# Kernel tuning notes

Hardware: AMD Instinct MI355X
Metric: run time of the kernel (lower is better)

The kernel has to match this reference:

```python
import jax, jax.numpy as jnp
import numpy as np

B = 16384   # batch
F = 26      # categorical fields
N = 100000  # rows per embedding table
M = 16      # embedding dim per field
NUM = 13    # numerical (dense) features
D = F * M + NUM  # embed_output_dim = 429
L = 6       # CrossNet layers (vector parameterization)
H = 1024    # MLP hidden


def setup_inputs() -> dict:
    key = jax.random.key(0)
    ks = jax.random.split(key, 10)
    Xi = jax.random.randint(ks[0], (B, F, 1), 0, N)
    Xv = jax.random.normal(ks[1], (B, NUM), dtype=jnp.float32)
    # per-field tables, init U(-sqrt(1/n), sqrt(1/n)) as in the torch code; stacked flat
    bound = float(np.sqrt(1.0 / N))
    emb_tables = jax.random.uniform(ks[2], (F * N, M), jnp.float32, -bound, bound)
    cross_w = jax.random.normal(ks[3], (L, D), dtype=jnp.float32) * 0.02
    cross_b = jnp.zeros((L, D), dtype=jnp.float32)
    W1 = jax.random.normal(ks[4], (D, H), dtype=jnp.float32) * (1.0 / np.sqrt(D))
    b1 = jnp.zeros((H,), dtype=jnp.float32)
    W2 = jax.random.normal(ks[5], (H, H), dtype=jnp.float32) * (1.0 / np.sqrt(H))
    b2 = jnp.zeros((H,), dtype=jnp.float32)
    Wout = jax.random.normal(ks[6], (H + D, 1), dtype=jnp.float32) * (1.0 / np.sqrt(H + D))
    bout = jnp.zeros((1,), dtype=jnp.float32)
    return dict(Xi=Xi, Xv=Xv, emb_tables=emb_tables, cross_w=cross_w,
                cross_b=cross_b, W1=W1, b1=b1, W2=W2, b2=b2, Wout=Wout, bout=bout)


def reference(Xi, Xv, emb_tables, cross_w, cross_b, W1, b1, W2, b2, Wout, bout):
    # Fused multi-table EmbeddingBag(mode='sum'): one gather over the stacked tables.
    offs = (jnp.arange(F, dtype=Xi.dtype) * N)[None, :, None]        # [1,F,1]
    flat_idx = (Xi + offs).reshape(-1)                               # [B*F*K]
    g = emb_tables[flat_idx].reshape(B, F, -1, M).sum(axis=2)        # [B,F,M] bag-sum
    x0 = jnp.concatenate([Xv, g.reshape(B, F * M)], axis=1)          # [B,D]
    # CrossNet, vector parameterization: x_{l+1} = x0 * (x_l . w_l) + b_l + x_l
    x = x0
    for l in range(L):
        xw = x @ cross_w[l]                                          # [B]
        x = x0 * xw[:, None] + cross_b[l] + x
    # Deep MLP on x0
    h = jax.nn.relu(x0 @ W1 + b1)
    h = jax.nn.relu(h @ W2 + b2)
    out = jnp.concatenate([h, x], axis=1) @ Wout + bout              # [B,1]
    return out[:, 0]
```

## Files before the change

kernel.cpp:

```cpp
#include <hip/hip_runtime.h>
#include <hip/hip_bf16.h>

#define B_   16384
#define F_   26
#define N_   100000
#define M_   16
#define NUM_ 13
#define D_   429
#define KP1_ 448
#define L_   6
#define H_   1024

typedef unsigned short u16;
typedef __bf16 bf16x8 __attribute__((ext_vector_type(8)));
typedef float  f32x4  __attribute__((ext_vector_type(4)));

__device__ __forceinline__ u16 f2bf_bits(float f) {
  union { float f; unsigned u; } x; x.f = f;
  unsigned r = x.u + 0x7FFFu + ((x.u >> 16) & 1u);
  return (u16)(r >> 16);
}

__global__ __launch_bounds__(256) void fused_front(
    const int* __restrict__ Xi, const float* __restrict__ Xv,
    const float* __restrict__ emb,
    const float* __restrict__ cw, const float* __restrict__ cb,
    const float* __restrict__ Wout, const float* __restrict__ bout,
    const float* __restrict__ W1, const float* __restrict__ W2,
    u16* __restrict__ x0b, u16* __restrict__ w1bt, u16* __restrict__ w2bt,
    float* __restrict__ out) {
  __shared__ __align__(16) u16 sbuf[4][KP1_];
  __shared__ __align__(16) float tile[64][68];
  const int blk = blockIdx.x;
  const int tid = threadIdx.x;
  if (blk < B_ / 4) {
    const int w = tid >> 6, lane = tid & 63;
    const int b = blk * 4 + w;
    const int* xi = Xi + b * F_;

    float x0r[7];
    #pragma unroll
    for (int i = 0; i < 7; ++i) {
      int e = i * 64 + lane;
      float v = 0.f;
      if (e < 416) {
        int f = e >> 4;
        int idx = xi[f];
        v = emb[((size_t)f * N_ + idx) * M_ + (e & 15)];
      } else if (e < D_) {
        v = Xv[b * NUM_ + (e - 416)];
      }
      x0r[i] = v;
      sbuf[w][e] = f2bf_bits(v);
    }

    float xr[7];
    #pragma unroll
    for (int i = 0; i < 7; ++i) xr[i] = x0r[i];
    for (int l = 0; l < L_; ++l) {
      float wl[7], bl[7];
      #pragma unroll
      for (int i = 0; i < 7; ++i) {
        int e = i * 64 + lane;
        if (e < D_) {
          int d = (e < 416) ? (13 + e) : (e - 416);
          wl[i] = cw[l * D_ + d]; bl[i] = cb[l * D_ + d];
        } else { wl[i] = 0.f; bl[i] = 0.f; }
      }
      float s = 0.f;
      #pragma unroll
      for (int i = 0; i < 7; ++i) s += xr[i] * wl[i];
      #pragma unroll
      for (int off = 32; off; off >>= 1) s += __shfl_xor(s, off);
      #pragma unroll
      for (int i = 0; i < 7; ++i) xr[i] = x0r[i] * s + bl[i] + xr[i];
    }

    __syncthreads();
    if (lane < 56)
      ((uint4*)(x0b + (size_t)b * KP1_))[lane] = ((const uint4*)sbuf[w])[lane];

    float s = 0.f;
    #pragma unroll
    for (int i = 0; i < 7; ++i) {
      int e = i * 64 + lane;
      if (e < D_) {
        int d = (e < 416) ? (13 + e) : (e - 416);
        s += xr[i] * Wout[H_ + d];
      }
    }
    #pragma unroll
    for (int off = 32; off; off >>= 1) s += __shfl_xor(s, off);
    if (lane == 0) out[b] = s + bout[0];
  } else {
    int pid = blk - B_ / 4;
    if (pid < 112) {
      const int ti = pid >> 4, tj = pid & 15;
      const int e0 = ti * 64, c0 = tj * 64;
      #pragma unroll
      for (int it = 0; it < 4; ++it) {
        int el = it * 16 + (tid >> 4);
        int e = e0 + el;
        int d = (e < 416) ? (13 + e) : ((e < D_) ? (e - 416) : -1);
        float4 v = make_float4(0.f, 0.f, 0.f, 0.f);
        if (d >= 0) v = *(const float4*)&W1[(size_t)d * H_ + c0 + (tid & 15) * 4];
        *(float4*)&tile[el][(tid & 15) * 4] = v;
      }
      __syncthreads();
      const int nl = tid >> 2, ks = (tid & 3) * 16;
      u16 tmp[16];
      #pragma unroll
      for (int x = 0; x < 16; ++x) tmp[x] = f2bf_bits(tile[ks + x][nl]);
      uint4* dst = (uint4*)&w1bt[(size_t)(c0 + nl) * KP1_ + e0 + ks];
      dst[0] = *(uint4*)&tmp[0];
      dst[1] = *(uint4*)&tmp[8];
    } else {
      pid -= 112;
      const int ti = pid >> 4, tj = pid & 15;
      const int k0 = ti * 64, c0 = tj * 64;
      #pragma unroll
      for (int it = 0; it < 4; ++it) {
        int kl = it * 16 + (tid >> 4);
        *(float4*)&tile[kl][(tid & 15) * 4] =
            *(const float4*)&W2[(size_t)(k0 + kl) * H_ + c0 + (tid & 15) * 4];
      }
      __syncthreads();
      const int nl = tid >> 2, ks = (tid & 3) * 16;
      u16 tmp[16];
      #pragma unroll
      for (int x = 0; x < 16; ++x) tmp[x] = f2bf_bits(tile[ks + x][nl]);
      uint4* dst = (uint4*)&w2bt[(size_t)(c0 + nl) * H_ + k0 + ks];
      dst[0] = *(uint4*)&tmp[0];
      dst[1] = *(uint4*)&tmp[8];
    }
  }
}

#define BARR __builtin_amdgcn_s_barrier()
#define VM6  asm volatile("s_waitcnt vmcnt(6)" ::: "memory")
#define VM0  asm volatile("s_waitcnt vmcnt(0)" ::: "memory")
#define MM(ACC) do { \
  __builtin_amdgcn_s_setprio(1); \
  _Pragma("unroll") \
  for (int mi = 0; mi < 4; ++mi) { \
    _Pragma("unroll") \
    for (int ni = 0; ni < 4; ++ni) \
      ACC[mi][ni] = __builtin_amdgcn_mfma_f32_16x16x32_bf16(af[mi], bfc[ni], ACC[mi][ni], 0, 0, 0); \
  } \
  __builtin_amdgcn_s_setprio(0); \
} while (0)

template<int MODE>
__global__ __launch_bounds__(512, 2) void gemm256(
    const u16* __restrict__ A, const u16* __restrict__ BT,
    const float* __restrict__ bias, u16* __restrict__ C,
    const float* __restrict__ Wout, float* __restrict__ out,
    int N, int K) {
  __shared__ __align__(16) u16 As[2][2][256 * 32];
  __shared__ __align__(16) u16 Bs[2][2][256 * 32];
  const int nbx = N >> 8;
  const int cpx = gridDim.x >> 3;
  const int swz = (blockIdx.x & 7) * cpx + (blockIdx.x >> 3);
  const int bx = swz % nbx;
  const int by = swz / nbx;
  const int tid = threadIdx.x;
  const int l = tid & 63;
  const int w = tid >> 6;
  const int wr = w >> 2, wc = w & 3;
  const int nkt = K >> 6;

  const int sr = tid >> 2;
  const int scs = ((tid & 3) ^ ((tid >> 3) & 3)) * 8;
  const u16* gA0 = A  + (size_t)(by * 256 + sr) * K + scs;
  const u16* gB0 = BT + (size_t)(bx * 256 + sr) * K + scs;
  const int dst0 = tid * 8;

  auto stgA = [&](int t, int kk) {
    const u16* s = gA0 + t * 64 + kk * 32;
    __builtin_amdgcn_global_load_lds(
        (const __attribute__((address_space(1))) void*)s,
        (__attribute__((address_space(3))) void*)&As[t & 1][kk][dst0], 16, 0, 0);
    __builtin_amdgcn_global_load_lds(
        (const __attribute__((address_space(1))) void*)(s + (size_t)128 * K),
        (__attribute__((address_space(3))) void*)&As[t & 1][kk][dst0 + 4096], 16, 0, 0);
  };
  auto stgB = [&](int t, int kk) {
    const u16* s = gB0 + t * 64 + kk * 32;
    __builtin_amdgcn_global_load_lds(
        (const __attribute__((address_space(1))) void*)s,
        (__attribute__((address_space(3))) void*)&Bs[t & 1][kk][dst0], 16, 0, 0);
    __builtin_amdgcn_global_load_lds(
        (const __attribute__((address_space(1))) void*)(s + (size_t)128 * K),
        (__attribute__((address_space(3))) void*)&Bs[t & 1][kk][dst0 + 4096], 16, 0, 0);
  };

  const int fr = l & 15, g = l >> 4;
  const int slot = (g ^ ((fr >> 1) & 3)) * 16;
  const int aoff = (wr * 128 + fr) * 64 + slot;
  const int boff = (wc * 64 + fr) * 64 + slot;

  bf16x8 af[4], bfc[4];
  auto rdA = [&](int buf, int kk, int mlo) {
    const char* base = (const char*)&As[buf][kk][0];
    #pragma unroll
    for (int m = 0; m < 4; ++m)
      af[m] = *(const bf16x8*)(base + aoff + (mlo + m) * 1024);
  };
  auto rdB = [&](int buf, int kk) {
    const char* base = (const char*)&Bs[buf][kk][0];
    #pragma unroll
    for (int n = 0; n < 4; ++n)
      bfc[n] = *(const bf16x8*)(base + boff + n * 1024);
  };

  f32x4 accLo[4][4] = {};
  f32x4 accHi[4][4] = {};

  stgA(0, 0); stgB(0, 0); stgA(0, 1); stgB(0, 1);
  stgA(1, 0); stgB(1, 0); stgB(1, 1);
  VM6;
  BARR;

  for (int t = 0; t < nkt; ++t) {
    const int buf = t & 1;
    const bool s1 = (t + 1 < nkt);
    const bool s2 = (t + 2 < nkt);
    rdA(buf, 0, 0); rdB(buf, 0);
    if (s1) stgA(t + 1, 1);
    BARR; MM(accLo); BARR;
    rdA(buf, 0, 4);
    if (s2) stgB(t + 2, 0);
    BARR; MM(accHi); BARR;
    rdA(buf, 1, 0); rdB(buf, 1);
    if (s2) stgA(t + 2, 0);
    BARR; MM(accLo); BARR;
    rdA(buf, 1, 4);
    if (s2) stgB(t + 2, 1);
    BARR; MM(accHi);
    if (s2)      { VM6; BARR; }
    else if (s1) { VM0; BARR; }
  }

  const int ccol0 = bx * 256 + wc * 64;
  const int row0 = by * 256 + wr * 128 + g * 4;
  if (MODE == 0) {
    #pragma unroll
    for (int n = 0; n < 4; ++n) {
      int col = ccol0 + n * 16 + fr;
      float bv = bias[col];
      #pragma unroll
      for (int m = 0; m < 4; ++m)
        #pragma unroll
        for (int r = 0; r < 4; ++r) {
          float v0 = fmaxf(accLo[m][n][r] + bv, 0.f);
          C[(size_t)(row0 + m * 16 + r) * N + col] = f2bf_bits(v0);
          float v1 = fmaxf(accHi[m][n][r] + bv, 0.f);
          C[(size_t)(row0 + 64 + m * 16 + r) * N + col] = f2bf_bits(v1);
        }
    }
  } else {
    float bv[4], wv[4];
    #pragma unroll
    for (int n = 0; n < 4; ++n) {
      int col = ccol0 + n * 16 + fr;
      bv[n] = bias[col]; wv[n] = Wout[col];
    }
    #pragma unroll
    for (int m = 0; m < 4; ++m)
      #pragma unroll
      for (int r = 0; r < 4; ++r) {
        float s0 = 0.f, s1v = 0.f;
        #pragma unroll
        for (int n = 0; n < 4; ++n) {
          s0  = fmaf(fmaxf(accLo[m][n][r] + bv[n], 0.f), wv[n], s0);
          s1v = fmaf(fmaxf(accHi[m][n][r] + bv[n], 0.f), wv[n], s1v);
        }
        s0 += __shfl_xor(s0, 1); s0 += __shfl_xor(s0, 2);
        s0 += __shfl_xor(s0, 4); s0 += __shfl_xor(s0, 8);
        s1v += __shfl_xor(s1v, 1); s1v += __shfl_xor(s1v, 2);
        s1v += __shfl_xor(s1v, 4); s1v += __shfl_xor(s1v, 8);
        if (fr == 0) {
          atomicAdd(out + row0 + m * 16 + r, s0);
          atomicAdd(out + row0 + 64 + m * 16 + r, s1v);
        }
      }
  }
}

extern "C" void kernel_launch(void* const* d_in, const int* in_sizes, int n_in,
                              void* d_out, int out_size, void* d_ws, size_t ws_size,
                              hipStream_t stream) {
  const int*   Xi   = (const int*)d_in[0];
  const float* Xv   = (const float*)d_in[1];
  const float* emb  = (const float*)d_in[2];
  const float* cw   = (const float*)d_in[3];
  const float* cb   = (const float*)d_in[4];
  const float* W1   = (const float*)d_in[5];
  const float* b1   = (const float*)d_in[6];
  const float* W2   = (const float*)d_in[7];
  const float* b2   = (const float*)d_in[8];
  const float* Wout = (const float*)d_in[9];
  const float* bout = (const float*)d_in[10];
  float* out = (float*)d_out;

  char* ws = (char*)d_ws;
  size_t off = 0;
  auto alloc = [&](size_t bytes) {
    void* p = ws + off; off += (bytes + 255) & ~(size_t)255; return p;
  };
  u16* x0b  = (u16*)alloc((size_t)B_ * KP1_ * 2);
  u16* w1bt = (u16*)alloc((size_t)H_ * KP1_ * 2);
  u16* w2bt = (u16*)alloc((size_t)H_ * H_ * 2);
  u16* h1   = (u16*)alloc((size_t)B_ * H_ * 2);

  hipLaunchKernelGGL(fused_front, dim3(B_ / 4 + 112 + 256), dim3(256), 0, stream,
                     Xi, Xv, emb, cw, cb, Wout, bout, W1, W2, x0b, w1bt, w2bt, out);
  hipLaunchKernelGGL((gemm256<0>), dim3((B_ / 256) * (H_ / 256)), dim3(512), 0, stream,
                     x0b, w1bt, b1, h1, nullptr, nullptr, H_, KP1_);
  hipLaunchKernelGGL((gemm256<1>), dim3((B_ / 256) * (H_ / 256)), dim3(512), 0, stream,
                     h1, w2bt, b2, nullptr, Wout, out, H_, H_);
}
```

Measured before the change: 95.01 us.

## Load GEMM B operand directly into registers, bypassing LDS staging

The GEMM no longer stages the B tile through shared memory. Each wave now loads its 64-column B fragments straight from global memory into registers, double-buffered across k-tiles, while A is still staged into LDS with direct global-to-LDS loads. The main loop is rewritten to issue one A stage plus the B register prefetch per k-tile, with fewer barriers and vmcnt(8) waits. This halves LDS footprint and removes the B LDS reads and writes, but both row-waves now fetch the same B data from global or L2. The extra B registers also raise register pressure under the 512-thread, 2-block launch bounds.

```diff
diff --git a/kernel.cpp b/kernel.cpp
--- a/kernel.cpp
+++ b/kernel.cpp
@@ -137,15 +137,15 @@
 }
 
 #define BARR __builtin_amdgcn_s_barrier()
-#define VM6  asm volatile("s_waitcnt vmcnt(6)" ::: "memory")
-#define VM0  asm volatile("s_waitcnt vmcnt(0)" ::: "memory")
-#define MM(ACC) do { \
+#define SBR  __builtin_amdgcn_sched_barrier(0)
+#define VM8  asm volatile("s_waitcnt vmcnt(8)" ::: "memory")
+#define MMQ(ACC, BB, KK) do { \
   __builtin_amdgcn_s_setprio(1); \
   _Pragma("unroll") \
   for (int mi = 0; mi < 4; ++mi) { \
     _Pragma("unroll") \
     for (int ni = 0; ni < 4; ++ni) \
-      ACC[mi][ni] = __builtin_amdgcn_mfma_f32_16x16x32_bf16(af[mi], bfc[ni], ACC[mi][ni], 0, 0, 0); \
+      ACC[mi][ni] = __builtin_amdgcn_mfma_f32_16x16x32_bf16(af[mi], BB[KK][ni], ACC[mi][ni], 0, 0, 0); \
   } \
   __builtin_amdgcn_s_setprio(0); \
 } while (0)
@@ -157,7 +157,6 @@
     const float* __restrict__ Wout, float* __restrict__ out,
     int N, int K) {
   __shared__ __align__(16) u16 As[2][2][256 * 32];
-  __shared__ __align__(16) u16 Bs[2][2][256 * 32];
   const int nbx = N >> 8;
   const int cpx = gridDim.x >> 3;
   const int swz = (blockIdx.x & 7) * cpx + (blockIdx.x >> 3);
@@ -171,74 +170,69 @@
 
   const int sr = tid >> 2;
   const int scs = ((tid & 3) ^ ((tid >> 3) & 3)) * 8;
-  const u16* gA0 = A  + (size_t)(by * 256 + sr) * K + scs;
-  const u16* gB0 = BT + (size_t)(bx * 256 + sr) * K + scs;
+  const u16* gA0 = A + (size_t)(by * 256 + sr) * K + scs;
   const int dst0 = tid * 8;
 
-  auto stgA = [&](int t, int kk) {
-    const u16* s = gA0 + t * 64 + kk * 32;
-    __builtin_amdgcn_global_load_lds(
-        (const __attribute__((address_space(1))) void*)s,
-        (__attribute__((address_space(3))) void*)&As[t & 1][kk][dst0], 16, 0, 0);
-    __builtin_amdgcn_global_load_lds(
-        (const __attribute__((address_space(1))) void*)(s + (size_t)128 * K),
-        (__attribute__((address_space(3))) void*)&As[t & 1][kk][dst0 + 4096], 16, 0, 0);
+  auto stgA = [&](int t) {
+    const u16* s = gA0 + t * 64;
+    #pragma unroll
+    for (int kk = 0; kk < 2; ++kk)
+      #pragma unroll
+      for (int i = 0; i < 2; ++i)
+        __builtin_amdgcn_global_load_lds(
+            (const __attribute__((address_space(1))) void*)(s + kk * 32 + (size_t)i * 128 * K),
+            (__attribute__((address_space(3))) void*)&As[t & 1][kk][dst0 + i * 4096], 16, 0, 0);
   };
-  auto stgB = [&](int t, int kk) {
-    const u16* s = gB0 + t * 64 + kk * 32;
-    __builtin_amdgcn_global_load_lds(
-        (const __attribute__((address_space(1))) void*)s,
-        (__attribute__((address_space(3))) void*)&Bs[t & 1][kk][dst0], 16, 0, 0);
-    __builtin_amdgcn_global_load_lds(
-        (const __attribute__((address_space(1))) void*)(s + (size_t)128 * K),
-        (__attribute__((address_space(3))) void*)&Bs[t & 1][kk][dst0 + 4096], 16, 0, 0);
+
+  const int fr = l & 15, g = l >> 4;
+  const u16* gBL = BT + (size_t)(bx * 256 + wc * 64 + fr) * K + g * 8;
+  auto loadB = [&](int t, bf16x8 (&bb)[2][4]) {
+    #pragma unroll
+    for (int kk = 0; kk < 2; ++kk)
+      #pragma unroll
+      for (int n = 0; n < 4; ++n)
+        bb[kk][n] = *(const bf16x8*)(gBL + (size_t)(n * 16) * K + t * 64 + kk * 32);
   };
 
-  const int fr = l & 15, g = l >> 4;
   const int slot = (g ^ ((fr >> 1) & 3)) * 16;
   const int aoff = (wr * 128 + fr) * 64 + slot;
-  const int boff = (wc * 64 + fr) * 64 + slot;
-
-  bf16x8 af[4], bfc[4];
+  bf16x8 af[4];
   auto rdA = [&](int buf, int kk, int mlo) {
     const char* base = (const char*)&As[buf][kk][0];
     #pragma unroll
     for (int m = 0; m < 4; ++m)
       af[m] = *(const bf16x8*)(base + aoff + (mlo + m) * 1024);
   };
-  auto rdB = [&](int buf, int kk) {
-    const char* base = (const char*)&Bs[buf][kk][0];
-    #pragma unroll
-    for (int n = 0; n < 4; ++n)
-      bfc[n] = *(const bf16x8*)(base + boff + n * 1024);
-  };
 
   f32x4 accLo[4][4] = {};
   f32x4 accHi[4][4] = {};
-
-  stgA(0, 0); stgB(0, 0); stgA(0, 1); stgB(0, 1);
-  stgA(1, 0); stgB(1, 0); stgB(1, 1);
-  VM6;
+  bf16x8 bE[2][4], bO[2][4];
+
+  stgA(0);
+  SBR;
+  loadB(0, bE);
+  VM8;
   BARR;
 
-  for (int t = 0; t < nkt; ++t) {
-    const int buf = t & 1;
-    const bool s1 = (t + 1 < nkt);
-    const bool s2 = (t + 2 < nkt);
-    rdA(buf, 0, 0); rdB(buf, 0);
-    if (s1) stgA(t + 1, 1);
-    BARR; MM(accLo); BARR;
-    rdA(buf, 0, 4);
-    if (s2) stgB(t + 2, 0);
-    BARR; MM(accHi); BARR;
-    rdA(buf, 1, 0); rdB(buf, 1);
-    if (s2) stgA(t + 2, 0);
-    BARR; MM(accLo); BARR;
-    rdA(buf, 1, 4);
-    if (s2) stgB(t + 2, 1);
-    BARR; MM(accHi);
-    if (s2)      { VM6; BARR; }
-    else if (s1) { VM0; BARR; }
+  for (int t = 0; t < nkt; t += 2) {
+    {
+      const bool s1 = (t + 1 < nkt);
+      if (s1) { stgA(t + 1); SBR; loadB(t + 1, bO); }
+      rdA(0, 0, 0); MMQ(accLo, bE, 0);
+      rdA(0, 0, 4); MMQ(accHi, bE, 0);
+      rdA(0, 1, 0); MMQ(accLo, bE, 1);
+      rdA(0, 1, 4); MMQ(accHi, bE, 1);
+      if (s1) { VM8; BARR; }
+    }
+    if (t + 1 < nkt) {
+      const bool s2 = (t + 2 < nkt);
+      if (s2) { stgA(t + 2); SBR; loadB(t + 2, bE); }
+      rdA(1, 0, 0); MMQ(accLo, bO, 0);
+      rdA(1, 0, 4); MMQ(accHi, bO, 0);
+      rdA(1, 1, 0); MMQ(accLo, bO, 1);
+      rdA(1, 1, 4); MMQ(accHi, bO, 1);
+      if (s2) { VM8; BARR; }
+    }
   }
 
   const int ccol0 = bx * 256 + wc * 64;
```

New measurement: 111.7 us. +17.6%, slower.
